# Performance work log

Hardware: AMD Instinct MI355X
Metric: run time of the kernel (lower is better)

Reference implementation:

```python
import jax, jax.numpy as jnp
import numpy as np

D_MODEL = 2048
NUM_Q_HEADS = 32
NUM_KV_HEADS = 8
HEAD_DIM = D_MODEL // NUM_Q_HEADS  # 64
DIM_KV = NUM_KV_HEADS * HEAD_DIM   # 512
ROPE_THETA = 500000.0
B, T = 1, 2048


def setup_inputs() -> dict:
    key = jax.random.key(0)
    ks = jax.random.split(key, 7)
    f = lambda k, shape, scale: (jax.random.normal(k, shape, jnp.float32) * scale)
    return {
        "q_embs": f(ks[0], (B, T, D_MODEL), 1.0),
        "k_embs": f(ks[1], (B, T, D_MODEL), 1.0),
        "v_embs": f(ks[2], (B, T, D_MODEL), 1.0),
        "w_q": f(ks[3], (D_MODEL, D_MODEL), 0.02),
        "w_k": f(ks[4], (D_MODEL, DIM_KV), 0.02),
        "w_v": f(ks[5], (D_MODEL, DIM_KV), 0.02),
        "w_o": f(ks[6], (D_MODEL, D_MODEL), 0.02),
    }


def _rope(x):
    # x: (B, H, T, D). Llama-style interleaved rotary embedding.
    Tn, D = x.shape[-2], x.shape[-1]
    inv_freq = 1.0 / (ROPE_THETA ** (jnp.arange(0, D, 2, dtype=jnp.float32) / D))  # (D/2,)
    ang = jnp.arange(Tn, dtype=jnp.float32)[:, None] * inv_freq[None, :]  # (T, D/2)
    cos, sin = jnp.cos(ang), jnp.sin(ang)
    x1, x2 = x[..., ::2], x[..., 1::2]
    # interleave rotated pairs back into last dim
    out = jnp.stack([x1 * cos - x2 * sin, x1 * sin + x2 * cos], axis=-1)
    return out.reshape(x.shape)


def reference(q_embs, k_embs, v_embs, w_q, w_k, w_v, w_o):
    Bn, Tn, _ = q_embs.shape
    # projections, then split heads: (B, T, H*D) -> (B, H, T, D)
    q = (q_embs @ w_q).reshape(Bn, Tn, NUM_Q_HEADS, HEAD_DIM).transpose(0, 2, 1, 3)
    k = (k_embs @ w_k).reshape(Bn, Tn, NUM_KV_HEADS, HEAD_DIM).transpose(0, 2, 1, 3)
    v = (v_embs @ w_v).reshape(Bn, Tn, NUM_KV_HEADS, HEAD_DIM).transpose(0, 2, 1, 3)
    q = _rope(q)
    k = _rope(k)
    # GQA: repeat each kv head n_rep consecutive times (matches torch expand+rearrange)
    n_rep = NUM_Q_HEADS // NUM_KV_HEADS
    k = jnp.repeat(k, n_rep, axis=1)
    v = jnp.repeat(v, n_rep, axis=1)
    scores = jnp.einsum("bhqd,bhkd->bhqk", q, k) * (HEAD_DIM ** -0.5)
    causal = jnp.tril(jnp.ones((Tn, Tn), dtype=bool))
    scores = jnp.where(causal, scores, -jnp.inf)
    wei = jax.nn.softmax(scores, axis=-1)
    out = jnp.einsum("bhqk,bhkd->bhqd", wei, v)
    out = out.transpose(0, 2, 1, 3).reshape(Bn, Tn, NUM_Q_HEADS * HEAD_DIM)
    return out @ w_o
```

## Files before the change

### kernel.cpp

```cpp
#include <hip/hip_runtime.h>
#include <hip/hip_bf16.h>
#include <cstdint>

#define D_MODEL 2048
#define T_SEQ   2048
#define NQH     32
#define NKVH    8
#define HD      64
#define DIM_KV  512

typedef __attribute__((ext_vector_type(8))) __bf16 bf16x8;
typedef __attribute__((ext_vector_type(4))) float  f32x4;
typedef __attribute__((ext_vector_type(4))) unsigned int u32x4;
typedef unsigned short ushort_t;

#define NEG_BIG (-1e30f)
#define AS1 __attribute__((address_space(1)))
#define AS3 __attribute__((address_space(3)))

__device__ __forceinline__ float bf2f(unsigned int u) {
    union { unsigned int i; float f; } v; v.i = u << 16; return v.f;
}
__device__ __forceinline__ ushort_t f2bf(float f) {
    __hip_bfloat16 h = __float2bfloat16(f);
    return *reinterpret_cast<ushort_t*>(&h);
}
__device__ __forceinline__ u32x4 pack8(f32x4 a, f32x4 b) {
    u32x4 r;
    r.x = (unsigned)f2bf(a.x) | ((unsigned)f2bf(a.y) << 16);
    r.y = (unsigned)f2bf(a.z) | ((unsigned)f2bf(a.w) << 16);
    r.z = (unsigned)f2bf(b.x) | ((unsigned)f2bf(b.y) << 16);
    r.w = (unsigned)f2bf(b.z) | ((unsigned)f2bf(b.w) << 16);
    return r;
}
__device__ __forceinline__ void gll16(const ushort_t* g, ushort_t* l) {
    __builtin_amdgcn_global_load_lds((const AS1 void*)g, (AS3 void*)l, 16, 0, 0);
}

__global__ __launch_bounds__(256) void transpose_w3(const float* __restrict__ Wq,
                                                    const float* __restrict__ Wk,
                                                    const float* __restrict__ Wv,
                                                    ushort_t* __restrict__ WqT,
                                                    ushort_t* __restrict__ WkT,
                                                    ushort_t* __restrict__ WvT) {
    __shared__ ushort_t tile[64][65];
    int bx = blockIdx.x;
    const float* W; ushort_t* Wt; int N, n0;
    if (bx < 32)      { W = Wq; Wt = WqT; N = 2048; n0 = bx * 64; }
    else if (bx < 40) { W = Wk; Wt = WkT; N = 512;  n0 = (bx - 32) * 64; }
    else              { W = Wv; Wt = WvT; N = 512;  n0 = (bx - 40) * 64; }
    const int K = 2048;
    int k0 = blockIdx.y * 64;
    int tid = threadIdx.x;
#pragma unroll
    for (int ii = 0; ii < 16; ii++) {
        int idx = tid + ii * 256;
        int r = idx >> 6, c = idx & 63;
        tile[r][c] = f2bf(W[(size_t)(k0 + r) * N + n0 + c]);
    }
    __syncthreads();
#pragma unroll
    for (int ii = 0; ii < 16; ii++) {
        int idx = tid + ii * 256;
        int r = idx >> 6, c = idx & 63;
        Wt[(size_t)(n0 + r) * K + k0 + c] = tile[c][r];
    }
}

__global__ __launch_bounds__(256) void transpose_w(const float* __restrict__ W,
                                                   ushort_t* __restrict__ Wt,
                                                   int K, int N) {
    __shared__ ushort_t tile[64][65];
    int n0 = blockIdx.x * 64;
    int k0 = blockIdx.y * 64;
    int tid = threadIdx.x;
#pragma unroll
    for (int ii = 0; ii < 16; ii++) {
        int idx = tid + ii * 256;
        int r = idx >> 6, c = idx & 63;
        tile[r][c] = f2bf(W[(size_t)(k0 + r) * N + n0 + c]);
    }
    __syncthreads();
#pragma unroll
    for (int ii = 0; ii < 16; ii++) {
        int idx = tid + ii * 256;
        int r = idx >> 6, c = idx & 63;
        Wt[(size_t)(n0 + r) * K + k0 + c] = tile[c][r];
    }
}

__global__ __launch_bounds__(256) void transpose_v(const ushort_t* __restrict__ V,
                                                   ushort_t* __restrict__ Vt) {
    __shared__ ushort_t tile[64][65];
    int h  = blockIdx.y;
    int j0 = blockIdx.x * 64;
    int tid = threadIdx.x;
#pragma unroll
    for (int ii = 0; ii < 16; ii++) {
        int idx = tid + ii * 256;
        int r = idx >> 6, c = idx & 63;
        tile[r][c] = V[(size_t)(j0 + r) * DIM_KV + h * HD + c];
    }
    __syncthreads();
#pragma unroll
    for (int ii = 0; ii < 16; ii++) {
        int idx = tid + ii * 256;
        int r = idx >> 6, c = idx & 63;
        Vt[((size_t)h * HD + r) * T_SEQ + j0 + c] = tile[c][r];
    }
}

__global__ __launch_bounds__(256, 6) void gemm_qkv(const float* __restrict__ Aq,
                                                   const float* __restrict__ Ak,
                                                   const float* __restrict__ Av,
                                                   const ushort_t* __restrict__ wqT,
                                                   const ushort_t* __restrict__ wkT,
                                                   const ushort_t* __restrict__ wvT,
                                                   ushort_t* __restrict__ Qb,
                                                   ushort_t* __restrict__ Kb,
                                                   ushort_t* __restrict__ Vb) {
    __shared__ ushort_t As[2][64][32];
    __shared__ ushort_t Bs[2][64][32];
    int tid  = threadIdx.x;
    int lane = tid & 63;
    int wave = tid >> 6;
    int bx   = blockIdx.x;
    const float* A; const ushort_t* Bt; ushort_t* C; int n0, ldc;
    if (bx < 32)      { A = Aq; Bt = wqT; C = Qb; n0 = bx * 64;        ldc = D_MODEL; }
    else if (bx < 40) { A = Ak; Bt = wkT; C = Kb; n0 = (bx - 32) * 64; ldc = DIM_KV; }
    else              { A = Av; Bt = wvT; C = Vb; n0 = (bx - 40) * 64; ldc = DIM_KV; }
    const int K = 2048;
    int m0 = blockIdx.y * 64;
    int wm = (wave >> 1) * 32;
    int wn = (wave & 1) * 32;
    int arow = tid >> 2;
    int acol = (tid & 3) * 8;

    f32x4 acc[2][2];
#pragma unroll
    for (int i = 0; i < 2; i++)
#pragma unroll
        for (int j = 0; j < 2; j++) acc[i][j] = (f32x4){0.f, 0.f, 0.f, 0.f};

    const int mrow = lane & 15;
    const int kq   = (lane >> 4) * 8;
    const float* Arow = A + (size_t)(m0 + arow) * K + acol;
    const ushort_t* Brow = Bt + (size_t)(n0 + arow) * K + acol;

    f32x4 pa0 = *(const f32x4*)(Arow);
    f32x4 pa1 = *(const f32x4*)(Arow + 4);
    gll16(Brow, &Bs[0][arow][acol]);
    *(u32x4*)&As[0][arow][acol] = pack8(pa0, pa1);
    __syncthreads();

    int cur = 0;
#pragma unroll 1
    for (int t = 0; t < 64; t++) {
        bool more = (t + 1) < 64;
        if (more) {
            int k1 = (t + 1) << 5;
            pa0 = *(const f32x4*)(Arow + k1);
            pa1 = *(const f32x4*)(Arow + k1 + 4);
            gll16(Brow + k1, &Bs[cur ^ 1][arow][acol]);
        }
        bf16x8 afr[2], bfr[2];
#pragma unroll
        for (int i = 0; i < 2; i++) afr[i] = *(const bf16x8*)&As[cur][wm + i * 16 + mrow][kq];
#pragma unroll
        for (int j = 0; j < 2; j++) bfr[j] = *(const bf16x8*)&Bs[cur][wn + j * 16 + mrow][kq];
#pragma unroll
        for (int i = 0; i < 2; i++)
#pragma unroll
            for (int j = 0; j < 2; j++)
                acc[i][j] = __builtin_amdgcn_mfma_f32_16x16x32_bf16(afr[i], bfr[j], acc[i][j], 0, 0, 0);
        if (more) {
            *(u32x4*)&As[cur ^ 1][arow][acol] = pack8(pa0, pa1);
        }
        __syncthreads();
        cur ^= 1;
    }

    int crow = (lane >> 4) * 4;
    int ccol = lane & 15;
#pragma unroll
    for (int i = 0; i < 2; i++)
#pragma unroll
        for (int j = 0; j < 2; j++) {
            int col = n0 + wn + j * 16 + ccol;
#pragma unroll
            for (int r = 0; r < 4; r++) {
                int row = m0 + wm + i * 16 + crow + r;
                C[(size_t)row * ldc + col] = f2bf(acc[i][j][r]);
            }
        }
}

template <int OF32>
__global__ __launch_bounds__(256) void gemm128x64(const ushort_t* __restrict__ A,
                                                  const ushort_t* __restrict__ Bt,
                                                  void* __restrict__ C,
                                                  int M, int N, int K) {
    __shared__ ushort_t As[2][128][32];
    __shared__ ushort_t Bs[2][64][32];
    int tid  = threadIdx.x;
    int lane = tid & 63;
    int wave = tid >> 6;
    int m0 = blockIdx.y * 128;
    int n0 = blockIdx.x * 64;
    int wm = (wave >> 1) * 64;
    int wn = (wave & 1) * 32;
    int lrow = tid >> 2;
    int lcol = (tid & 3) * 8;

    f32x4 acc[4][2];
#pragma unroll
    for (int i = 0; i < 4; i++)
#pragma unroll
        for (int j = 0; j < 2; j++) acc[i][j] = (f32x4){0.f, 0.f, 0.f, 0.f};

    const int mrow = lane & 15;
    const int kq   = (lane >> 4) * 8;

    gll16(A  + (size_t)(m0 + lrow) * K + lcol,      &As[0][lrow][lcol]);
    gll16(A  + (size_t)(m0 + 64 + lrow) * K + lcol, &As[0][64 + lrow][lcol]);
    gll16(Bt + (size_t)(n0 + lrow) * K + lcol,      &Bs[0][lrow][lcol]);
    __syncthreads();

    int nk  = K >> 5;
    int cur = 0;
    for (int t = 0; t < nk; t++) {
        if (t + 1 < nk) {
            int k1 = (t + 1) << 5;
            gll16(A  + (size_t)(m0 + lrow) * K + k1 + lcol,      &As[cur ^ 1][lrow][lcol]);
            gll16(A  + (size_t)(m0 + 64 + lrow) * K + k1 + lcol, &As[cur ^ 1][64 + lrow][lcol]);
            gll16(Bt + (size_t)(n0 + lrow) * K + k1 + lcol,      &Bs[cur ^ 1][lrow][lcol]);
        }
        bf16x8 afr[4], bfr[2];
#pragma unroll
        for (int i = 0; i < 4; i++) afr[i] = *(const bf16x8*)&As[cur][wm + i * 16 + mrow][kq];
#pragma unroll
        for (int j = 0; j < 2; j++) bfr[j] = *(const bf16x8*)&Bs[cur][wn + j * 16 + mrow][kq];
#pragma unroll
        for (int i = 0; i < 4; i++)
#pragma unroll
            for (int j = 0; j < 2; j++)
                acc[i][j] = __builtin_amdgcn_mfma_f32_16x16x32_bf16(afr[i], bfr[j], acc[i][j], 0, 0, 0);
        __syncthreads();
        cur ^= 1;
    }

    int crow = (lane >> 4) * 4;
    int ccol = lane & 15;
#pragma unroll
    for (int i = 0; i < 4; i++)
#pragma unroll
        for (int j = 0; j < 2; j++) {
            int col = n0 + wn + j * 16 + ccol;
#pragma unroll
            for (int r = 0; r < 4; r++) {
                int row = m0 + wm + i * 16 + crow + r;
                if (OF32) ((float*)C)[(size_t)row * N + col] = acc[i][j][r];
                else      ((ushort_t*)C)[(size_t)row * N + col] = f2bf(acc[i][j][r]);
            }
        }
}

__global__ void rope_fused(ushort_t* __restrict__ Qb, ushort_t* __restrict__ Kb) {
    const int NQ = T_SEQ * (D_MODEL / 2);
    const int NK = T_SEQ * (DIM_KV / 2);
    int idx = blockIdx.x * blockDim.x + threadIdx.x;
    ushort_t* X; int cols;
    if (idx < NQ) { X = Qb; cols = D_MODEL; }
    else {
        idx -= NQ;
        if (idx >= NK) return;
        X = Kb; cols = DIM_KV;
    }
    int ppr = cols >> 1;
    int t = idx / ppr;
    int j = idx - t * ppr;
    int i = j & 31;
    int col = ((j >> 5) << 6) + (i << 1);
    float inv = expf(-(float)i * (13.122363377404328f / 32.0f));
    float ang = (float)t * inv;
    float c = cosf(ang), s = sinf(ang);
    size_t base = (size_t)t * cols + col;
    float x1 = bf2f((unsigned int)X[base]);
    float x2 = bf2f((unsigned int)X[base + 1]);
    X[base]     = f2bf(x1 * c - x2 * s);
    X[base + 1] = f2bf(x1 * s + x2 * c);
}

__global__ __launch_bounds__(256) void attn_mfma(const ushort_t* __restrict__ Q,
                                                 const ushort_t* __restrict__ Kb,
                                                 const ushort_t* __restrict__ Vt,
                                                 ushort_t* __restrict__ Ob) {
    __shared__ ushort_t Qs[64][72];
    __shared__ ushort_t Ks[64][72];
    __shared__ ushort_t Vs[64][72];
    __shared__ ushort_t Ps[64][72];

    int tid  = threadIdx.x;
    int lane = tid & 63;
    int wave = tid >> 6;
    int h    = blockIdx.x;
    int hk   = h >> 2;
    int y    = blockIdx.y;
    int qt   = (y < 8) ? y : (y < 16) ? 23 - y : (y < 24) ? y : 55 - y;
    int q0   = qt * 64;
    int l15  = lane & 15;
    int quad = lane >> 4;
    int kq   = quad * 8;

    int r = tid >> 3;
    int c = (tid & 7) * 8;

    *(u32x4*)&Qs[r][c]      = *(const u32x4*)(Q + (size_t)(q0 + r) * D_MODEL + h * HD + c);
    *(u32x4*)&Qs[r + 32][c] = *(const u32x4*)(Q + (size_t)(q0 + r + 32) * D_MODEL + h * HD + c);
    __syncthreads();
    bf16x8 aq0 = *(const bf16x8*)&Qs[wave * 16 + l15][kq];
    bf16x8 aq1 = *(const bf16x8*)&Qs[wave * 16 + l15][kq + 32];

    f32x4 oacc[4];
    float l_i[4];
#pragma unroll
    for (int i = 0; i < 4; i++) {
        oacc[i] = (f32x4){0.f, 0.f, 0.f, 0.f};
        l_i[i] = 0.f;
    }

    u32x4 kr0, kr1, vr0, vr1;
    {
        kr0 = *(const u32x4*)(Kb + (size_t)(0 + r) * DIM_KV + hk * HD + c);
        kr1 = *(const u32x4*)(Kb + (size_t)(32 + r) * DIM_KV + hk * HD + c);
        vr0 = *(const u32x4*)(Vt + ((size_t)hk * HD + r) * T_SEQ + 0 + c);
        vr1 = *(const u32x4*)(Vt + ((size_t)hk * HD + r + 32) * T_SEQ + 0 + c);
    }

    int ntiles = qt + 1;
    for (int jt = 0; jt < ntiles; jt++) {
        __syncthreads();
        *(u32x4*)&Ks[r][c]      = kr0;
        *(u32x4*)&Ks[r + 32][c] = kr1;
        *(u32x4*)&Vs[r][c]      = vr0;
        *(u32x4*)&Vs[r + 32][c] = vr1;
        __syncthreads();
        if (jt + 1 < ntiles) {
            int j0 = (jt + 1) * 64;
            kr0 = *(const u32x4*)(Kb + (size_t)(j0 + r) * DIM_KV + hk * HD + c);
            kr1 = *(const u32x4*)(Kb + (size_t)(j0 + r + 32) * DIM_KV + hk * HD + c);
            vr0 = *(const u32x4*)(Vt + ((size_t)hk * HD + r) * T_SEQ + j0 + c);
            vr1 = *(const u32x4*)(Vt + ((size_t)hk * HD + r + 32) * T_SEQ + j0 + c);
        }

        f32x4 sacc[4];
#pragma unroll
        for (int ct = 0; ct < 4; ct++) {
            bf16x8 bk0 = *(const bf16x8*)&Ks[ct * 16 + l15][kq];
            bf16x8 bk1 = *(const bf16x8*)&Ks[ct * 16 + l15][kq + 32];
            sacc[ct] = __builtin_amdgcn_mfma_f32_16x16x32_bf16(aq0, bk0, (f32x4){0.f,0.f,0.f,0.f}, 0, 0, 0);
            sacc[ct] = __builtin_amdgcn_mfma_f32_16x16x32_bf16(aq1, bk1, sacc[ct], 0, 0, 0);
        }

        bool diag = (jt == ntiles - 1);
#pragma unroll
        for (int reg = 0; reg < 4; reg++) {
            int y2 = quad * 4 + reg;
            float sum = 0.f;
#pragma unroll
            for (int ct = 0; ct < 4; ct++) {
                float sv = sacc[ct][reg] * 0.125f;
                if (diag && (ct * 16 + l15 > wave * 16 + y2)) sv = NEG_BIG;
                float p = __expf(sv);
                sum += p;
                Ps[wave * 16 + y2][ct * 16 + l15] = f2bf(p);
            }
            l_i[reg] += sum;
        }

        bf16x8 ap0 = *(const bf16x8*)&Ps[wave * 16 + l15][kq];
        bf16x8 ap1 = *(const bf16x8*)&Ps[wave * 16 + l15][kq + 32];
#pragma unroll
        for (int dt = 0; dt < 4; dt++) {
            bf16x8 bv0 = *(const bf16x8*)&Vs[dt * 16 + l15][kq];
            bf16x8 bv1 = *(const bf16x8*)&Vs[dt * 16 + l15][kq + 32];
            oacc[dt] = __builtin_amdgcn_mfma_f32_16x16x32_bf16(ap0, bv0, oacc[dt], 0, 0, 0);
            oacc[dt] = __builtin_amdgcn_mfma_f32_16x16x32_bf16(ap1, bv1, oacc[dt], 0, 0, 0);
        }
    }

#pragma unroll
    for (int reg = 0; reg < 4; reg++) {
        float tot = l_i[reg];
#pragma unroll
        for (int off = 1; off < 16; off <<= 1) tot += __shfl_xor(tot, off, 64);
        float inv = (tot > 0.f) ? 1.0f / tot : 0.f;
        int row = q0 + wave * 16 + quad * 4 + reg;
#pragma unroll
        for (int dt = 0; dt < 4; dt++) {
            Ob[(size_t)row * D_MODEL + h * HD + dt * 16 + l15] = f2bf(oacc[dt][reg] * inv);
        }
    }
}

extern "C" void kernel_launch(void* const* d_in, const int* in_sizes, int n_in,
                              void* d_out, int out_size, void* d_ws, size_t ws_size,
                              hipStream_t stream) {
    const float* q_embs = (const float*)d_in[0];
    const float* k_embs = (const float*)d_in[1];
    const float* v_embs = (const float*)d_in[2];
    const float* w_q = (const float*)d_in[3];
    const float* w_k = (const float*)d_in[4];
    const float* w_v = (const float*)d_in[5];
    const float* w_o = (const float*)d_in[6];
    float* out = (float*)d_out;

    const size_t M1 = (size_t)1024 * 1024;
    ushort_t* base = (ushort_t*)d_ws;
    ushort_t* wqT = base + 0 * M1;
    ushort_t* woT = base + 0 * M1;
    ushort_t* wkT = base + 4 * M1;
    ushort_t* Vt  = base + 4 * M1;
    ushort_t* wvT = base + 5 * M1;
    ushort_t* Qb  = base + 6 * M1;
    ushort_t* Kb  = base + 10 * M1;
    ushort_t* Vb  = base + 11 * M1;
    ushort_t* Ab  = base + 12 * M1;

    dim3 blk(256);

    transpose_w3<<<dim3(48, 32), blk, 0, stream>>>(w_q, w_k, w_v, wqT, wkT, wvT);

    gemm_qkv<<<dim3(48, 32), blk, 0, stream>>>(q_embs, k_embs, v_embs,
                                               wqT, wkT, wvT, Qb, Kb, Vb);

    const int NROPE = T_SEQ * (D_MODEL / 2) + T_SEQ * (DIM_KV / 2);
    rope_fused<<<(NROPE + 255) / 256, blk, 0, stream>>>(Qb, Kb);

    transpose_v<<<dim3(32, 8), blk, 0, stream>>>(Vb, Vt);
    transpose_w<<<dim3(32, 32), blk, 0, stream>>>(w_o, woT, 2048, 2048);

    attn_mfma<<<dim3(32, 32), blk, 0, stream>>>(Qb, Kb, Vt, Ab);

    gemm128x64<1><<<dim3(32, 16), blk, 0, stream>>>(Ab, woT, out, 2048, 2048, 2048);
}
```

Before: 304.3 us.

## Pre-convert embeddings to bf16 and remap QKV GEMM blocks for locality

Adds a conv3 kernel that converts the three fp32 embedding inputs to bf16 once, so gemm_qkv can load both A and B tiles with direct global-to-LDS loads instead of reading fp32 and packing in registers. The QKV GEMM grid is flattened to 1D with a block remap that groups tiles into bands, likely aimed at XCD/L2 locality. Workspace is reorganized, with wqT and Qb staged in the output buffer. This adds an extra pass over 3x16MB of fp32 input, and the GEMM re-reads the embeddings as bf16.

```diff
diff --git a/kernel.cpp b/kernel.cpp
--- a/kernel.cpp
+++ b/kernel.cpp
@@ -35,6 +35,19 @@
 }
 __device__ __forceinline__ void gll16(const ushort_t* g, ushort_t* l) {
     __builtin_amdgcn_global_load_lds((const AS1 void*)g, (AS3 void*)l, 16, 0, 0);
+}
+
+__global__ __launch_bounds__(256) void conv3(const float* __restrict__ Xq,
+                                             const float* __restrict__ Xk,
+                                             const float* __restrict__ Xv,
+                                             ushort_t* __restrict__ E) {
+    int which = blockIdx.y;
+    const float* X = (which == 0) ? Xq : (which == 1) ? Xk : Xv;
+    ushort_t* out = E + (size_t)which * (4u * 1024 * 1024);
+    int i8 = (blockIdx.x * 256 + threadIdx.x) * 8;
+    f32x4 a = *(const f32x4*)(X + i8);
+    f32x4 b = *(const f32x4*)(X + i8 + 4);
+    *(u32x4*)(out + i8) = pack8(a, b);
 }
 
 __global__ __launch_bounds__(256) void transpose_w3(const float* __restrict__ Wq,
@@ -110,31 +123,44 @@
     }
 }
 
-__global__ __launch_bounds__(256, 6) void gemm_qkv(const float* __restrict__ Aq,
-                                                   const float* __restrict__ Ak,
-                                                   const float* __restrict__ Av,
-                                                   const ushort_t* __restrict__ wqT,
-                                                   const ushort_t* __restrict__ wkT,
-                                                   const ushort_t* __restrict__ wvT,
-                                                   ushort_t* __restrict__ Qb,
-                                                   ushort_t* __restrict__ Kb,
-                                                   ushort_t* __restrict__ Vb) {
+__global__ __launch_bounds__(256) void gemm_qkv(const ushort_t* __restrict__ Eq,
+                                                const ushort_t* __restrict__ Ek,
+                                                const ushort_t* __restrict__ Ev,
+                                                const ushort_t* __restrict__ wqT,
+                                                const ushort_t* __restrict__ wkT,
+                                                const ushort_t* __restrict__ wvT,
+                                                ushort_t* __restrict__ Qb,
+                                                ushort_t* __restrict__ Kb,
+                                                ushort_t* __restrict__ Vb) {
     __shared__ ushort_t As[2][64][32];
     __shared__ ushort_t Bs[2][64][32];
     int tid  = threadIdx.x;
     int lane = tid & 63;
     int wave = tid >> 6;
-    int bx   = blockIdx.x;
-    const float* A; const ushort_t* Bt; ushort_t* C; int n0, ldc;
-    if (bx < 32)      { A = Aq; Bt = wqT; C = Qb; n0 = bx * 64;        ldc = D_MODEL; }
-    else if (bx < 40) { A = Ak; Bt = wkT; C = Kb; n0 = (bx - 32) * 64; ldc = DIM_KV; }
-    else              { A = Av; Bt = wvT; C = Vb; n0 = (bx - 40) * 64; ldc = DIM_KV; }
+
+    int b = blockIdx.x;
+    int L = (b & 7) * 192 + (b >> 3);
+    const ushort_t *A, *Bt; ushort_t* C; int m, n, ldc;
+    if (L < 1024) {
+        int band = L >> 8, r = L & 255;
+        n = r >> 3; m = (band << 3) + (r & 7);
+        A = Eq; Bt = wqT; C = Qb; ldc = D_MODEL;
+    } else if (L < 1280) {
+        int LK = L - 1024; int band = LK >> 6, r = LK & 63;
+        n = r >> 3; m = (band << 3) + (r & 7);
+        A = Ek; Bt = wkT; C = Kb; ldc = DIM_KV;
+    } else {
+        int LV = L - 1280; int band = LV >> 6, r = LV & 63;
+        n = r >> 3; m = (band << 3) + (r & 7);
+        A = Ev; Bt = wvT; C = Vb; ldc = DIM_KV;
+    }
     const int K = 2048;
-    int m0 = blockIdx.y * 64;
+    int m0 = m * 64;
+    int n0 = n * 64;
     int wm = (wave >> 1) * 32;
     int wn = (wave & 1) * 32;
-    int arow = tid >> 2;
-    int acol = (tid & 3) * 8;
+    int lrow = tid >> 2;
+    int lcol = (tid & 3) * 8;
 
     f32x4 acc[2][2];
 #pragma unroll
@@ -144,24 +170,20 @@
 
     const int mrow = lane & 15;
     const int kq   = (lane >> 4) * 8;
-    const float* Arow = A + (size_t)(m0 + arow) * K + acol;
-    const ushort_t* Brow = Bt + (size_t)(n0 + arow) * K + acol;
-
-    f32x4 pa0 = *(const f32x4*)(Arow);
-    f32x4 pa1 = *(const f32x4*)(Arow + 4);
-    gll16(Brow, &Bs[0][arow][acol]);
-    *(u32x4*)&As[0][arow][acol] = pack8(pa0, pa1);
+    const ushort_t* Arow = A  + (size_t)(m0 + lrow) * K + lcol;
+    const ushort_t* Brow = Bt + (size_t)(n0 + lrow) * K + lcol;
+
+    gll16(Arow, &As[0][lrow][lcol]);
+    gll16(Brow, &Bs[0][lrow][lcol]);
     __syncthreads();
 
     int cur = 0;
 #pragma unroll 1
     for (int t = 0; t < 64; t++) {
-        bool more = (t + 1) < 64;
-        if (more) {
+        if (t + 1 < 64) {
             int k1 = (t + 1) << 5;
-            pa0 = *(const f32x4*)(Arow + k1);
-            pa1 = *(const f32x4*)(Arow + k1 + 4);
-            gll16(Brow + k1, &Bs[cur ^ 1][arow][acol]);
+            gll16(Arow + k1, &As[cur ^ 1][lrow][lcol]);
+            gll16(Brow + k1, &Bs[cur ^ 1][lrow][lcol]);
         }
         bf16x8 afr[2], bfr[2];
 #pragma unroll
@@ -173,9 +195,6 @@
 #pragma unroll
             for (int j = 0; j < 2; j++)
                 acc[i][j] = __builtin_amdgcn_mfma_f32_16x16x32_bf16(afr[i], bfr[j], acc[i][j], 0, 0, 0);
-        if (more) {
-            *(u32x4*)&As[cur ^ 1][arow][acol] = pack8(pa0, pa1);
-        }
         __syncthreads();
         cur ^= 1;
     }
@@ -417,22 +436,27 @@
 
     const size_t M1 = (size_t)1024 * 1024;
     ushort_t* base = (ushort_t*)d_ws;
-    ushort_t* wqT = base + 0 * M1;
-    ushort_t* woT = base + 0 * M1;
-    ushort_t* wkT = base + 4 * M1;
-    ushort_t* Vt  = base + 4 * M1;
-    ushort_t* wvT = base + 5 * M1;
-    ushort_t* Qb  = base + 6 * M1;
-    ushort_t* Kb  = base + 10 * M1;
-    ushort_t* Vb  = base + 11 * M1;
-    ushort_t* Ab  = base + 12 * M1;
+    ushort_t* Eq  = base + 0 * M1;
+    ushort_t* Ek  = base + 4 * M1;
+    ushort_t* Ev  = base + 8 * M1;
+    ushort_t* wkT = base + 12 * M1;
+    ushort_t* wvT = base + 13 * M1;
+    ushort_t* Kb  = base + 14 * M1;
+    ushort_t* Vb  = base + 15 * M1;
+    ushort_t* Vt  = base + 0 * M1;
+    ushort_t* woT = base + 1 * M1;
+    ushort_t* Ab  = base + 5 * M1;
+    ushort_t* wqT = (ushort_t*)d_out;
+    ushort_t* Qb  = (ushort_t*)d_out + 4 * M1;
 
     dim3 blk(256);
 
     transpose_w3<<<dim3(48, 32), blk, 0, stream>>>(w_q, w_k, w_v, wqT, wkT, wvT);
 
-    gemm_qkv<<<dim3(48, 32), blk, 0, stream>>>(q_embs, k_embs, v_embs,
-                                               wqT, wkT, wvT, Qb, Kb, Vb);
+    conv3<<<dim3(2048, 3), blk, 0, stream>>>(q_embs, k_embs, v_embs, Eq);
+
+    gemm_qkv<<<dim3(1536), blk, 0, stream>>>(Eq, Ek, Ev, wqT, wkT, wvT,
+                                             Qb, Kb, Vb);
 
     const int NROPE = T_SEQ * (D_MODEL / 2) + T_SEQ * (DIM_KV / 2);
     rope_fused<<<(NROPE + 255) / 256, blk, 0, stream>>>(Qb, Kb);
```

After: 275.5 us. 9.5% less time.
